# Kernel tuning notes

Hardware: AMD Instinct MI355X
Metric: run time of the kernel (lower is better)

The kernel has to match this reference:

```python
import jax, jax.numpy as jnp
from jax import lax
import numpy as np

B, W, M, F = 8, 20, 512, 16
H = 128          # n_hidden
HALF = 64        # half_hid
K = 10           # conv out channels
LONG_K = W // 2  # dilated conv kernel


def setup_inputs() -> dict:
    key = jax.random.key(0)
    ks = jax.random.split(key, 24)
    s = 0.1  # weight scale (xavier-ish)
    return {
        "X": jax.random.normal(ks[0], (B, W, M, F), jnp.float32),
        "Y": jax.random.uniform(ks[1], (B, M), jnp.float32),
        "adj": jax.random.uniform(ks[2], (M, M), jnp.float32),
        "V": jax.random.normal(ks[3], (HALF,), jnp.float32) * s,
        "bv": jax.random.normal(ks[4], (1,), jnp.float32) * s,
        "W1": jax.random.normal(ks[5], (HALF, H), jnp.float32) * s,
        "b1": jax.random.normal(ks[6], (HALF,), jnp.float32) * s,
        "W2": jax.random.normal(ks[7], (HALF, H), jnp.float32) * s,
        "Wb": jax.random.normal(ks[8], (M, M), jnp.float32) * s,
        "wb": jax.random.normal(ks[9], (1,), jnp.float32) * s,
        "conv_w": jax.random.normal(ks[10], (K, F, W), jnp.float32) * s,
        "conv_b": jax.random.normal(ks[11], (K,), jnp.float32) * s,
        "convl_w": jax.random.normal(ks[12], (K, F, LONG_K), jnp.float32) * s,
        "convl_b": jax.random.normal(ks[13], (K,), jnp.float32) * s,
        "gru_Wih": jax.random.normal(ks[14], (3 * H, F), jnp.float32) * s,
        "gru_Whh": jax.random.normal(ks[15], (3 * H, H), jnp.float32) * s,
        "gru_bih": jax.random.normal(ks[16], (3 * H,), jnp.float32) * s,
        "gru_bhh": jax.random.normal(ks[17], (3 * H,), jnp.float32) * s,
        "gc1_W": jax.random.normal(ks[18], (3 * K, H), jnp.float32) * s,
        "gc1_b": jax.random.normal(ks[19], (H,), jnp.float32) * s,
        "gc2_W": jax.random.normal(ks[20], (H, K), jnp.float32) * s,
        "gc2_b": jax.random.normal(ks[21], (K,), jnp.float32) * s,
        "out_W": jax.random.normal(ks[22], (1, H + K), jnp.float32) * s,
        "out_b": jax.random.normal(ks[23], (1,), jnp.float32) * s,
    }


def _gru_last(xseq, Wih, Whh, bih, bhh):
    # xseq: (N, T, F) -> last hidden (N, H), PyTorch GRU gate order r,z,n
    n_hid = Whh.shape[1]
    def step(h, x_t):
        gx = x_t @ Wih.T + bih
        gh = h @ Whh.T + bhh
        xr, xz, xn = jnp.split(gx, 3, axis=-1)
        hr, hz, hn = jnp.split(gh, 3, axis=-1)
        r = jax.nn.sigmoid(xr + hr)
        z = jax.nn.sigmoid(xz + hz)
        n = jnp.tanh(xn + r * hn)
        return (1.0 - z) * n + z * h, None
    h0 = jnp.zeros((xseq.shape[0], n_hid), xseq.dtype)
    hT, _ = lax.scan(step, h0, jnp.moveaxis(xseq, 1, 0))
    return hT


def _forward(X, Y, adj, V, bv, W1, b1, W2, Wb, wb, conv_w, conv_b, convl_w,
             convl_b, gru_Wih, gru_Whh, gru_bih, gru_bhh, gc1_W, gc1_b,
             gc2_W, gc2_b, out_W, out_b):
    b, w, m, f = X.shape
    # ---- temporal branch: GRU per node ----
    x = jnp.transpose(X, (0, 2, 1, 3)).reshape(b * m, w, f)
    last_hid = _gru_last(x, gru_Wih, gru_Whh, gru_bih, gru_bhh).reshape(b, m, -1)
    out_temporal = last_hid
    # ---- attention-style adaptive adjacency ----
    # hid_rpt_m[b,i,j]=last_hid[b,j]; hid_rpt_w[b,i,j]=last_hid[b,i]
    p1 = jnp.einsum('bjh,kh->bjk', last_hid, W1)  # pairs with column index j
    p2 = jnp.einsum('bih,kh->bik', last_hid, W2)  # pairs with row index i
    pre = p1[:, None, :, :] + p2[:, :, None, :] + b1  # (b,m,m,half)
    a_mx = jnp.einsum('bijk,k->bij', jax.nn.elu(pre), V) + bv[0]
    # F.normalize(p=2, dim=1)
    nrm = jnp.sqrt(jnp.sum(a_mx * a_mx, axis=1, keepdims=True))
    a_mx = a_mx / jnp.maximum(nrm, 1e-12)
    # ---- per-node conv1d (vectorized over nodes) ----
    Xc = jnp.transpose(X, (0, 2, 3, 1)).reshape(b * m, f, w)  # (bm, f, w)
    dn = ('NCH', 'OIH', 'NCH')
    r = lax.conv_general_dilated(Xc, conv_w, (1,), 'VALID', dimension_numbers=dn)
    r = r + conv_b[None, :, None]                      # (bm, K, 1)
    rl = lax.conv_general_dilated(Xc, convl_w, (1,), 'VALID',
                                  rhs_dilation=(2,), dimension_numbers=dn)
    rl = rl + convl_b[None, :, None]                   # (bm, K, long_out)
    r_cat = jnp.concatenate([r, rl], axis=-1)          # (bm, K, 1+long_out)
    r_l = jax.nn.relu(r_cat.reshape(b, m, -1))         # (b, m, (1+long_out)*K)
    # ---- gate learned adjacency with fixed adjacency ----
    c = jax.nn.sigmoid(jnp.einsum('bij,jk->bik', a_mx, Wb) + wb[0])
    A = adj[None] * c + a_mx * (1.0 - c)               # (b,m,m)
    # ---- graph convolutions: out = A @ (x @ W) + b ----
    h1 = jax.nn.relu(jnp.einsum('bij,bjh->bih', A, r_l @ gc1_W) + gc1_b)
    out_spatial = jax.nn.relu(jnp.einsum('bij,bjh->bih', A, h1 @ gc2_W) + gc2_b)
    # ---- readout ----
    out = jnp.concatenate([out_spatial, out_temporal], axis=-1)
    out = (out @ out_W.T + out_b).squeeze(-1)          # (b, m)
    y = out.reshape(-1)
    Yf = Y.reshape(-1)
    # BCE with logits: softplus(y) - Y*y, averaged
    loss = jnp.mean(jax.nn.softplus(y) - Yf * y)
    return loss, jax.nn.sigmoid(y)


def reference(X, Y, adj, V, bv, W1, b1, W2, Wb, wb, conv_w, conv_b, convl_w,
              convl_b, gru_Wih, gru_Whh, gru_bih, gru_bhh, gc1_W, gc1_b,
              gc2_W, gc2_b, out_W, out_b):
    return _forward(X, Y, adj, V, bv, W1, b1, W2, Wb, wb, conv_w, conv_b,
                    convl_w, convl_b, gru_Wih, gru_Whh, gru_bih, gru_bhh,
                    gc1_W, gc1_b, gc2_W, gc2_b, out_W, out_b)
```

## Files before the change

kernel.cpp:

```cpp
#include <hip/hip_runtime.h>
#include <math.h>

#define Bn 8
#define Wn 20
#define Mn 512
#define Fn 16
#define Hn 128
#define HALFn 64
#define Kn 10

typedef __attribute__((ext_vector_type(8))) short short8;
typedef __attribute__((ext_vector_type(4))) float f32x4;
typedef unsigned short ushort_t;

__device__ __forceinline__ float sigmoidf_(float x) {
  return 1.0f / (1.0f + __expf(-x));
}
__device__ __forceinline__ float tanhf_(float x) {
  float xx = fminf(fmaxf(x, -15.f), 15.f);
  float e = __expf(2.f * xx);
  return (e - 1.f) / (e + 1.f);
}
__device__ __forceinline__ float reluf_(float x) { return fmaxf(x, 0.f); }
__device__ __forceinline__ float eluf_(float x) {
  return (x > 0.f) ? x : (__expf(x) - 1.f);
}
__device__ __forceinline__ ushort_t bf16_rne(float v) {
  unsigned u = __float_as_uint(v);
  u += 0x7FFFu + ((u >> 16) & 1u);
  return (ushort_t)(u >> 16);
}
__device__ __forceinline__ float bf16_to_f(ushort_t b) {
  return __uint_as_float(((unsigned)b) << 16);
}

__global__ __launch_bounds__(256) void pack_kernel(
    const float* __restrict__ Whh, const float* __restrict__ Wih,
    const float* __restrict__ Wb, ushort_t* __restrict__ Bpack,
    ushort_t* __restrict__ WbT_hi, ushort_t* __restrict__ WbT_lo,
    float* __restrict__ ssq, float* __restrict__ d_out) {
  int tid = threadIdx.x;
  if (blockIdx.x < 240) {
    int idx = blockIdx.x * 256 + tid;
    if (idx < 4096) ssq[idx] = 0.f;
    if (idx == 0) d_out[0] = 0.f;
    if (idx >= 24 * 5 * 512) return;
    int j = idx & 7;
    int lane = (idx >> 3) & 63;
    int ks = (idx >> 9) % 5;
    int nt = idx / (5 * 512);
    int k = ks * 32 + (lane >> 4) * 8 + j;
    int g = (nt & 7) * 16 + (nt >> 3) * 128 + (lane & 15);
    float val = 0.f;
    if (k < 128) val = Whh[g * 128 + k];
    else if (k < 144) val = Wih[g * 16 + (k - 128)];
    ushort_t hb = bf16_rne(val);
    float lo = val - bf16_to_f(hb);
    Bpack[(((long)nt * 5 + ks) * 2 + 0) * 512 + lane * 8 + j] = hb;
    Bpack[(((long)nt * 5 + ks) * 2 + 1) * 512 + lane * 8 + j] = bf16_rne(lo);
  } else {
    int t = blockIdx.x - 240;
    int k0 = (t >> 3) * 64, j0 = (t & 7) * 64;
    __shared__ float wt[64][65];
    for (int idx = tid; idx < 4096; idx += 256) {
      int r = idx >> 6, c = idx & 63;
      wt[r][c] = Wb[(long)(k0 + r) * 512 + j0 + c];
    }
    __syncthreads();
    for (int idx = tid; idx < 4096; idx += 256) {
      int r = idx >> 6, c = idx & 63;
      float v = wt[c][r];
      ushort_t hb = bf16_rne(v);
      WbT_hi[(long)(j0 + r) * 512 + k0 + c] = hb;
      WbT_lo[(long)(j0 + r) * 512 + k0 + c] = bf16_rne(v - bf16_to_f(hb));
    }
  }
}

#define LDK 168
#define HSZ (16 * LDK)
__global__ __launch_bounds__(512, 1) void gru_kernel(
    const float* __restrict__ X, const ushort_t* __restrict__ Bpack,
    const float* __restrict__ bih, const float* __restrict__ bhh,
    const float* __restrict__ W1, const float* __restrict__ W2,
    const float* __restrict__ b1, float* __restrict__ last_hid,
    float* __restrict__ p1, float* __restrict__ p2) {
  const int tid = threadIdx.x;
  const int wave = tid >> 6;
  const int lane = tid & 63;
  const int quad = lane >> 4;
  const int jl = lane & 15;
  const int j0 = wave * 16;
  const int blk = blockIdx.x;
  const int b = blk >> 5;
  const int m0 = (blk & 31) * 16;

  __shared__ __align__(16) ushort_t smem_hs[4 * HSZ];

  short8 frR[5][2], frZ[5][2], frN[4][2], frXN[2];
#pragma unroll
  for (int ks = 0; ks < 5; ++ks) {
#pragma unroll
    for (int p = 0; p < 2; ++p) {
      frR[ks][p] = *(const short8*)&Bpack[(((long)(wave) * 5 + ks) * 2 + p) * 512 + lane * 8];
      frZ[ks][p] = *(const short8*)&Bpack[(((long)(8 + wave) * 5 + ks) * 2 + p) * 512 + lane * 8];
    }
  }
#pragma unroll
  for (int ks = 0; ks < 4; ++ks) {
#pragma unroll
    for (int p = 0; p < 2; ++p)
      frN[ks][p] = *(const short8*)&Bpack[(((long)(16 + wave) * 5 + ks) * 2 + p) * 512 + lane * 8];
  }
#pragma unroll
  for (int p = 0; p < 2; ++p)
    frXN[p] = *(const short8*)&Bpack[(((long)(16 + wave) * 5 + 4) * 2 + p) * 512 + lane * 8];

  const float cr  = bih[j0 + jl] + bhh[j0 + jl];
  const float cz  = bih[128 + j0 + jl] + bhh[128 + j0 + jl];
  const float cnx = bih[256 + j0 + jl];
  const float cnh = bhh[256 + j0 + jl];

  for (int i = tid; i < 4 * HSZ; i += 512) smem_hs[i] = 0;

  const float* Xb = X + (long)b * (Wn * Mn * Fn) + (long)m0 * Fn;
  float x0 = 0.f;
  if (tid < 256) x0 = Xb[tid];
  __syncthreads();
  if (tid < 256) {
    int s = tid >> 4, f = tid & 15;
    ushort_t hb = bf16_rne(x0);
    smem_hs[0 * HSZ + s * LDK + 128 + f] = hb;
    smem_hs[2 * HSZ + s * LDK + 128 + f] = bf16_rne(x0 - bf16_to_f(hb));
  }
  __syncthreads();

  float hp[4] = {0.f, 0.f, 0.f, 0.f};

  for (int t = 0; t < Wn; ++t) {
    const int cur = t & 1, nxt = cur ^ 1;
    const int hiC = cur * HSZ, loC = (2 + cur) * HSZ;
    const int hiN = nxt * HSZ, loN = (2 + nxt) * HSZ;
    float xpre = 0.f;
    if (tid < 256 && t < Wn - 1) xpre = Xb[(long)(t + 1) * (Mn * Fn) + tid];

    f32x4 aR[2], aZ[2], aHN[2], aXN;
    aR[0] = aR[1] = aZ[0] = aZ[1] = aHN[0] = aHN[1] = aXN = (f32x4){0.f, 0.f, 0.f, 0.f};
#pragma unroll
    for (int ks = 0; ks < 5; ++ks) {
      const int p = ks & 1;
      short8 ah = *(const short8*)&smem_hs[hiC + jl * LDK + ks * 32 + quad * 8];
      short8 al = *(const short8*)&smem_hs[loC + jl * LDK + ks * 32 + quad * 8];
      aR[p] = __builtin_amdgcn_mfma_f32_16x16x32_bf16(ah, frR[ks][0], aR[p], 0, 0, 0);
      aR[p] = __builtin_amdgcn_mfma_f32_16x16x32_bf16(ah, frR[ks][1], aR[p], 0, 0, 0);
      aR[p] = __builtin_amdgcn_mfma_f32_16x16x32_bf16(al, frR[ks][0], aR[p], 0, 0, 0);
      aZ[p] = __builtin_amdgcn_mfma_f32_16x16x32_bf16(ah, frZ[ks][0], aZ[p], 0, 0, 0);
      aZ[p] = __builtin_amdgcn_mfma_f32_16x16x32_bf16(ah, frZ[ks][1], aZ[p], 0, 0, 0);
      aZ[p] = __builtin_amdgcn_mfma_f32_16x16x32_bf16(al, frZ[ks][0], aZ[p], 0, 0, 0);
      if (ks < 4) {
        aHN[p] = __builtin_amdgcn_mfma_f32_16x16x32_bf16(ah, frN[ks][0], aHN[p], 0, 0, 0);
        aHN[p] = __builtin_amdgcn_mfma_f32_16x16x32_bf16(ah, frN[ks][1], aHN[p], 0, 0, 0);
        aHN[p] = __builtin_amdgcn_mfma_f32_16x16x32_bf16(al, frN[ks][0], aHN[p], 0, 0, 0);
      } else {
        aXN = __builtin_amdgcn_mfma_f32_16x16x32_bf16(ah, frXN[0], aXN, 0, 0, 0);
        aXN = __builtin_amdgcn_mfma_f32_16x16x32_bf16(ah, frXN[1], aXN, 0, 0, 0);
        aXN = __builtin_amdgcn_mfma_f32_16x16x32_bf16(al, frXN[0], aXN, 0, 0, 0);
      }
    }

#pragma unroll
    for (int reg = 0; reg < 4; ++reg) {
      float r = sigmoidf_(aR[0][reg] + aR[1][reg] + cr);
      float z = sigmoidf_(aZ[0][reg] + aZ[1][reg] + cz);
      float n = tanhf_(aXN[reg] + cnx + r * (aHN[0][reg] + aHN[1][reg] + cnh));
      float h = (1.f - z) * n + z * hp[reg];
      hp[reg] = h;
      int s = quad * 4 + reg;
      ushort_t hb = bf16_rne(h);
      smem_hs[hiN + s * LDK + j0 + jl] = hb;
      smem_hs[loN + s * LDK + j0 + jl] = bf16_rne(h - bf16_to_f(hb));
    }
    if (tid < 256 && t < Wn - 1) {
      int s = tid >> 4, f = tid & 15;
      ushort_t hb = bf16_rne(xpre);
      smem_hs[hiN + s * LDK + 128 + f] = hb;
      smem_hs[loN + s * LDK + 128 + f] = bf16_rne(xpre - bf16_to_f(hb));
    }
    __syncthreads();
  }

  float* hs_f = (float*)smem_hs;
#pragma unroll
  for (int reg = 0; reg < 4; ++reg) {
    int s = quad * 4 + reg;
    float h = hp[reg];
    last_hid[(long)(blk * 16 + s) * Hn + j0 + jl] = h;
    hs_f[s * 132 + j0 + jl] = h;
  }
  __syncthreads();
  {
    int k = tid & 63;
    int part = (tid >> 6) & 1;
    int sg = tid >> 7;
    const float* Wp = part ? W2 : W1;
    float a[4];
    float init = part ? 0.f : b1[k];
    a[0] = a[1] = a[2] = a[3] = init;
    for (int h = 0; h < 128; h += 4) {
      float4 w = *(const float4*)&Wp[k * 128 + h];
#pragma unroll
      for (int rr = 0; rr < 4; ++rr) {
        float4 q = *(const float4*)&hs_f[(sg * 4 + rr) * 132 + h];
        a[rr] += q.x * w.x + q.y * w.y + q.z * w.z + q.w * w.w;
      }
    }
    float* outp = part ? p2 : p1;
#pragma unroll
    for (int rr = 0; rr < 4; ++rr)
      outp[(long)(blk * 16 + sg * 4 + rr) * 64 + k] = a[rr];
  }
}

__global__ __launch_bounds__(128) void conv_t1_kernel(
    const float* __restrict__ X, const float* __restrict__ conv_w,
    const float* __restrict__ conv_b, const float* __restrict__ convl_w,
    const float* __restrict__ convl_b, const float* __restrict__ gc1_W,
    ushort_t* __restrict__ t1T_hi, ushort_t* __restrict__ t1T_lo) {
  int tid = threadIdx.x;
  int n0 = blockIdx.x * 8;
  int b = n0 >> 9, m0 = n0 & 511;
  __shared__ float xs[8][16][20];
  __shared__ float cw[3200];
  __shared__ float clw[1600];
  __shared__ float rs[8][32];
  for (int idx = tid; idx < 3200; idx += 128) cw[idx] = conv_w[idx];
  for (int idx = tid; idx < 1600; idx += 128) clw[idx] = convl_w[idx];
  for (int w = 0; w < 20; ++w)
    xs[tid >> 4][tid & 15][w] = X[((long)(b * 20 + w) * 512 + m0) * 16 + tid];
  __syncthreads();
  if (tid < 80) {
    int s = tid / 10, k = tid % 10;
    float a0 = conv_b[k];
    float l0 = convl_b[k], l1 = convl_b[k];
    for (int f = 0; f < 16; ++f) {
#pragma unroll
      for (int w = 0; w < 20; ++w) a0 = fmaf(xs[s][f][w], cw[k * 320 + f * 20 + w], a0);
#pragma unroll
      for (int q = 0; q < 10; ++q) {
        float wv = clw[k * 160 + f * 10 + q];
        l0 = fmaf(xs[s][f][2 * q], wv, l0);
        l1 = fmaf(xs[s][f][2 * q + 1], wv, l1);
      }
    }
    rs[s][k * 3 + 0] = reluf_(a0);
    rs[s][k * 3 + 1] = reluf_(l0);
    rs[s][k * 3 + 2] = reluf_(l1);
  }
  __syncthreads();
  float w[30];
#pragma unroll
  for (int q = 0; q < 30; ++q) w[q] = gc1_W[q * 128 + tid];
  long base = ((long)b * 128 + tid) * 512 + m0;
#pragma unroll
  for (int s = 0; s < 8; ++s) {
    float a = 0.f;
#pragma unroll
    for (int q = 0; q < 30; ++q) a = fmaf(rs[s][q], w[q], a);
    ushort_t hb = bf16_rne(a);
    t1T_hi[base + s] = hb;
    t1T_lo[base + s] = bf16_rne(a - bf16_to_f(hb));
  }
}

__global__ __launch_bounds__(256) void amx_kernel(
    const float* __restrict__ p1, const float* __restrict__ p2,
    const float* __restrict__ V, const float* __restrict__ bv,
    float* __restrict__ amx, float* __restrict__ ssq) {
  int tid = threadIdx.x;
  int j0 = blockIdx.x * 32, i0 = blockIdx.y * 32, bz = blockIdx.z;
  __shared__ float p1s[32][68];
  __shared__ float p2s[32][68];
  __shared__ float Vs[64];
  __shared__ float cred[16][33];
  if (tid < 64) Vs[tid] = V[tid];
  {
    int rr = tid >> 3, c0 = (tid & 7) * 8;
    *(float4*)&p1s[rr][c0]     = *(const float4*)&p1[(long)(bz * 512 + j0 + rr) * 64 + c0];
    *(float4*)&p1s[rr][c0 + 4] = *(const float4*)&p1[(long)(bz * 512 + j0 + rr) * 64 + c0 + 4];
    *(float4*)&p2s[rr][c0]     = *(const float4*)&p2[(long)(bz * 512 + i0 + rr) * 64 + c0];
    *(float4*)&p2s[rr][c0 + 4] = *(const float4*)&p2[(long)(bz * 512 + i0 + rr) * 64 + c0 + 4];
  }
  __syncthreads();
  int r0 = tid >> 4, c0 = tid & 15;
  float acc[2][2] = {{0.f, 0.f}, {0.f, 0.f}};
  for (int k = 0; k < 64; ++k) {
    float vj0 = p1s[c0][k], vj1 = p1s[c0 + 16][k];
    float vi0 = p2s[r0][k], vi1 = p2s[r0 + 16][k];
    float vk = Vs[k];
    acc[0][0] = fmaf(eluf_(vj0 + vi0), vk, acc[0][0]);
    acc[0][1] = fmaf(eluf_(vj1 + vi0), vk, acc[0][1]);
    acc[1][0] = fmaf(eluf_(vj0 + vi1), vk, acc[1][0]);
    acc[1][1] = fmaf(eluf_(vj1 + vi1), vk, acc[1][1]);
  }
  float bvv = bv[0];
  float s2[2] = {0.f, 0.f};
#pragma unroll
  for (int a = 0; a < 2; ++a)
#pragma unroll
    for (int c = 0; c < 2; ++c) {
      float v = acc[a][c] + bvv;
      amx[((long)(bz * 512 + i0 + r0 + a * 16)) * 512 + j0 + c0 + c * 16] = v;
      s2[c] += v * v;
    }
  cred[r0][c0] = s2[0];
  cred[r0][c0 + 16] = s2[1];
  __syncthreads();
  if (tid < 32) {
    float s = 0.f;
#pragma unroll
    for (int p = 0; p < 16; ++p) s += cred[p][tid];
    atomicAdd(&ssq[bz * 512 + j0 + tid], s);
  }
}

#define CPK 40
__global__ __launch_bounds__(256, 2) void gemm_cA(
    const float* __restrict__ amx, const ushort_t* __restrict__ WbT_hi,
    const ushort_t* __restrict__ WbT_lo, const float* __restrict__ adj,
    const float* __restrict__ wb, const float* __restrict__ ssq,
    float* __restrict__ A) {
  const int bz = blockIdx.z;
  const int i0 = blockIdx.y * 64;
  const int j0 = blockIdx.x * 64;
  const int tid = threadIdx.x;
  const int wave = tid >> 6;
  const int lane = tid & 63;
  const int quad = lane >> 4, jl = lane & 15;
  const int wm = (wave & 1) * 32, wn = (wave >> 1) * 32;

  __shared__ __align__(16) ushort_t Ahi[64][CPK];
  __shared__ __align__(16) ushort_t Alo[64][CPK];
  __shared__ __align__(16) ushort_t Bhi[64][CPK];
  __shared__ __align__(16) ushort_t Blo[64][CPK];
  __shared__ float rs_s[512];

  const float* Abase = amx + (long)bz * 262144;
  const float* sb = ssq + bz * 512;
  for (int i = tid; i < 512; i += 256)
    rs_s[i] = 1.f / fmaxf(sqrtf(sb[i]), 1e-12f);

  f32x4 acc[2][2];
#pragma unroll
  for (int a = 0; a < 2; ++a)
#pragma unroll
    for (int c = 0; c < 2; ++c) acc[a][c] = (f32x4){0.f, 0.f, 0.f, 0.f};

  for (int kk0 = 0; kk0 < 512; kk0 += 32) {
    __syncthreads();
#pragma unroll
    for (int l = 0; l < 2; ++l) {
      int e = l * 1024 + tid * 4;
      int r = e >> 5, kq = e & 31;
      float4 v = *(const float4*)&Abase[(long)(i0 + r) * 512 + kk0 + kq];
      float4 sc = *(const float4*)&rs_s[kk0 + kq];
      float vv[4] = {v.x * sc.x, v.y * sc.y, v.z * sc.z, v.w * sc.w};
#pragma unroll
      for (int q = 0; q < 4; ++q) {
        ushort_t hb = bf16_rne(vv[q]);
        Ahi[r][kq + q] = hb;
        Alo[r][kq + q] = bf16_rne(vv[q] - bf16_to_f(hb));
      }
    }
    {
      int r = tid >> 2, kc = (tid & 3) * 8;
      *(uint4*)&Bhi[r][kc] = *(const uint4*)&WbT_hi[(long)(j0 + r) * 512 + kk0 + kc];
      *(uint4*)&Blo[r][kc] = *(const uint4*)&WbT_lo[(long)(j0 + r) * 512 + kk0 + kc];
    }
    __syncthreads();
    short8 ah[2], al[2], bh[2], bl[2];
#pragma unroll
    for (int tm = 0; tm < 2; ++tm) {
      ah[tm] = *(const short8*)&Ahi[wm + tm * 16 + jl][quad * 8];
      al[tm] = *(const short8*)&Alo[wm + tm * 16 + jl][quad * 8];
    }
#pragma unroll
    for (int tn = 0; tn < 2; ++tn) {
      bh[tn] = *(const short8*)&Bhi[wn + tn * 16 + jl][quad * 8];
      bl[tn] = *(const short8*)&Blo[wn + tn * 16 + jl][quad * 8];
    }
#pragma unroll
    for (int tm = 0; tm < 2; ++tm)
#pragma unroll
      for (int tn = 0; tn < 2; ++tn) {
        acc[tm][tn] = __builtin_amdgcn_mfma_f32_16x16x32_bf16(ah[tm], bh[tn], acc[tm][tn], 0, 0, 0);
        acc[tm][tn] = __builtin_amdgcn_mfma_f32_16x16x32_bf16(ah[tm], bl[tn], acc[tm][tn], 0, 0, 0);
        acc[tm][tn] = __builtin_amdgcn_mfma_f32_16x16x32_bf16(al[tm], bh[tn], acc[tm][tn], 0, 0, 0);
      }
  }

  const float wbv = wb[0];
#pragma unroll
  for (int tn = 0; tn < 2; ++tn) {
    int j = j0 + wn + tn * 16 + jl;
    float sj = rs_s[j];
#pragma unroll
    for (int tm = 0; tm < 2; ++tm) {
#pragma unroll
      for (int reg = 0; reg < 4; ++reg) {
        int i = i0 + wm + tm * 16 + quad * 4 + reg;
        long ofs = (long)bz * 262144 + (long)i * 512 + j;
        float c = sigmoidf_(acc[tm][tn][reg] + wbv);
        float am = Abase[(long)i * 512 + j] * sj;
        float ad = adj[(long)i * 512 + j];
        A[ofs] = ad * c + am * (1.f - c);
      }
    }
  }
}

__global__ __launch_bounds__(512, 1) void gemm_h1t2(
    const float* __restrict__ A, const ushort_t* __restrict__ t1T_hi,
    const ushort_t* __restrict__ t1T_lo, const float* __restrict__ gc1_b,
    const float* __restrict__ gc2_W, float* __restrict__ t2) {
  const int bz = blockIdx.y;
  const int i0 = blockIdx.x * 16;
  const int tid = threadIdx.x;
  const int wave = tid >> 6;
  const int lane = tid & 63;
  const int quad = lane >> 4, jl = lane & 15;

  __shared__ __align__(16) ushort_t Ahi[16][CPK];
  __shared__ __align__(16) ushort_t Alo[16][CPK];
  __shared__ __align__(16) ushort_t Bhi[128][CPK];
  __shared__ __align__(16) ushort_t Blo[128][CPK];
  __shared__ float h1s[16][132];
  __shared__ float gw[1280];

  const float* Ab = A + (long)bz * 262144;
  for (int idx = tid; idx < 1280; idx += 512) gw[idx] = gc2_W[idx];

  f32x4 acc = {0.f, 0.f, 0.f, 0.f};

  for (int kk0 = 0; kk0 < 512; kk0 += 32) {
    __syncthreads();
    {
      int r = tid >> 5, kq = tid & 31;
      float v = Ab[(long)(i0 + r) * 512 + kk0 + kq];
      ushort_t hb = bf16_rne(v);
      Ahi[r][kq] = hb;
      Alo[r][kq] = bf16_rne(v - bf16_to_f(hb));
    }
    {
      int r = tid >> 2, kc = (tid & 3) * 8;
      *(uint4*)&Bhi[r][kc] = *(const uint4*)&t1T_hi[((long)bz * 128 + r) * 512 + kk0 + kc];
      *(uint4*)&Blo[r][kc] = *(const uint4*)&t1T_lo[((long)bz * 128 + r) * 512 + kk0 + kc];
    }
    __syncthreads();
    short8 ah = *(const short8*)&Ahi[jl][quad * 8];
    short8 al = *(const short8*)&Alo[jl][quad * 8];
    short8 bh = *(const short8*)&Bhi[wave * 16 + jl][quad * 8];
    short8 bl = *(const short8*)&Blo[wave * 16 + jl][quad * 8];
    acc = __builtin_amdgcn_mfma_f32_16x16x32_bf16(ah, bh, acc, 0, 0, 0);
    acc = __builtin_amdgcn_mfma_f32_16x16x32_bf16(ah, bl, acc, 0, 0, 0);
    acc = __builtin_amdgcn_mfma_f32_16x16x32_bf16(al, bh, acc, 0, 0, 0);
  }
  __syncthreads();
  {
    int n = wave * 16 + jl;
    float bb = gc1_b[n];
#pragma unroll
    for (int reg = 0; reg < 4; ++reg) {
      int r = quad * 4 + reg;
      h1s[r][n] = reluf_(acc[reg] + bb);
    }
  }
  __syncthreads();
  if (tid < 160) {
    int r = tid / 10, c = tid % 10;
    float a = 0.f;
#pragma unroll 4
    for (int k = 0; k < 128; ++k) a = fmaf(h1s[r][k], gw[k * 10 + c], a);
    t2[((long)bz * 512 + i0 + r) * 10 + c] = a;
  }
}

__global__ __launch_bounds__(256) void spat_readout(
    const float* __restrict__ A, const float* __restrict__ t2,
    const float* __restrict__ gc2_b, const float* __restrict__ last_hid,
    const float* __restrict__ out_W, const float* __restrict__ out_b,
    const float* __restrict__ Y, float* __restrict__ d_out) {
  int tid = threadIdx.x;
  int bz = blockIdx.y;
  int i0 = blockIdx.x * 8;
  __shared__ float t2s[5120];
  __shared__ float wS[138];
  __shared__ float osps[8][12];
  for (int idx = tid; idx < 5120; idx += 256) t2s[idx] = t2[(long)bz * 5120 + idx];
  for (int idx = tid; idx < 138; idx += 256) wS[idx] = out_W[idx];
  __syncthreads();
  int r = tid >> 5, sk = tid & 31;
  const float* Arow = A + (long)bz * 262144 + (long)(i0 + r) * 512;
  float acc[10] = {0, 0, 0, 0, 0, 0, 0, 0, 0, 0};
  for (int k = sk; k < 512; k += 32) {
    float av = Arow[k];
    const float* tp = &t2s[k * 10];
#pragma unroll
    for (int c = 0; c < 10; ++c) acc[c] = fmaf(av, tp[c], acc[c]);
  }
#pragma unroll
  for (int off = 16; off; off >>= 1)
#pragma unroll
    for (int c = 0; c < 10; ++c) acc[c] += __shfl_xor(acc[c], off);
  if (sk == 0) {
#pragma unroll
    for (int c = 0; c < 10; ++c) osps[r][c] = reluf_(acc[c] + gc2_b[c]);
  }
  __syncthreads();
  float l = 0.f;
  if (tid < 8) {
    int gid = bz * 512 + i0 + tid;
    float y = out_b[0];
#pragma unroll
    for (int k = 0; k < 10; ++k) y = fmaf(osps[tid][k], wS[k], y);
    const float* hp = &last_hid[(long)gid * 128];
    for (int h = 0; h < 128; h += 4) {
      float4 hv = *(const float4*)&hp[h];
      y = fmaf(hv.x, wS[10 + h + 0], y);
      y = fmaf(hv.y, wS[10 + h + 1], y);
      y = fmaf(hv.z, wS[10 + h + 2], y);
      y = fmaf(hv.w, wS[10 + h + 3], y);
    }
    d_out[1 + gid] = sigmoidf_(y);
    l = fmaxf(y, 0.f) + log1pf(__expf(-fabsf(y))) - Y[gid] * y;
  }
  if (tid < 64) {
#pragma unroll
    for (int off = 4; off; off >>= 1) l += __shfl_down(l, off);
    if (tid == 0) atomicAdd(d_out, l * (1.0f / 4096.f));
  }
}

extern "C" void kernel_launch(void* const* d_in, const int* in_sizes, int n_in,
                              void* d_out, int out_size, void* d_ws, size_t ws_size,
                              hipStream_t stream) {
  const float* X       = (const float*)d_in[0];
  const float* Y       = (const float*)d_in[1];
  const float* adj     = (const float*)d_in[2];
  const float* V       = (const float*)d_in[3];
  const float* bv      = (const float*)d_in[4];
  const float* W1      = (const float*)d_in[5];
  const float* b1      = (const float*)d_in[6];
  const float* W2      = (const float*)d_in[7];
  const float* Wb      = (const float*)d_in[8];
  const float* wb      = (const float*)d_in[9];
  const float* conv_w  = (const float*)d_in[10];
  const float* conv_b  = (const float*)d_in[11];
  const float* convl_w = (const float*)d_in[12];
  const float* convl_b = (const float*)d_in[13];
  const float* gWih    = (const float*)d_in[14];
  const float* gWhh    = (const float*)d_in[15];
  const float* gbih    = (const float*)d_in[16];
  const float* gbhh    = (const float*)d_in[17];
  const float* gc1_W   = (const float*)d_in[18];
  const float* gc1_b   = (const float*)d_in[19];
  const float* gc2_W   = (const float*)d_in[20];
  const float* gc2_b   = (const float*)d_in[21];
  const float* out_W   = (const float*)d_in[22];
  const float* out_b   = (const float*)d_in[23];
  float* out = (float*)d_out;

  float* ws = (float*)d_ws;
  float* lhid  = ws; ws += 524288;
  float* p1    = ws; ws += 262144;
  float* p2    = ws; ws += 262144;
  float* amx   = ws; ws += 2097152;
  float* ssq   = ws; ws += 4096;
  float* Abuf  = ws; ws += 2097152;
  float* t2    = ws; ws += 40960;
  float* Bpkf  = ws; ws += 122880;
  float* WbTf  = ws; ws += 262144;
  float* t1Tf  = ws; ws += 524288;
  if (ws_size < (size_t)(ws - (float*)d_ws) * sizeof(float)) return;
  ushort_t* Bpack  = (ushort_t*)Bpkf;
  ushort_t* WbT_hi = (ushort_t*)WbTf;
  ushort_t* WbT_lo = WbT_hi + 262144;
  ushort_t* t1T_hi = (ushort_t*)t1Tf;
  ushort_t* t1T_lo = t1T_hi + 524288;

  pack_kernel<<<304, 256, 0, stream>>>(gWhh, gWih, Wb, Bpack, WbT_hi, WbT_lo,
                                       ssq, out);
  gru_kernel<<<256, 512, 0, stream>>>(X, Bpack, gbih, gbhh, W1, W2, b1,
                                      lhid, p1, p2);
  conv_t1_kernel<<<512, 128, 0, stream>>>(X, conv_w, conv_b, convl_w, convl_b,
                                          gc1_W, t1T_hi, t1T_lo);
  amx_kernel<<<dim3(16, 16, 8), 256, 0, stream>>>(p1, p2, V, bv, amx, ssq);
  gemm_cA<<<dim3(8, 8, 8), 256, 0, stream>>>(amx, WbT_hi, WbT_lo, adj, wb,
                                             ssq, Abuf);
  gemm_h1t2<<<dim3(32, 8), 512, 0, stream>>>(Abuf, t1T_hi, t1T_lo, gc1_b,
                                             gc2_W, t2);
  spat_readout<<<dim3(64, 8), 256, 0, stream>>>(Abuf, t2, gc2_b, lhid,
                                                out_W, out_b, Y, out);
}
```

Before: 256.1 us.

## Fuse pack, conv and amx kernels; pack GRU weight fragments inside the GRU kernel

Drops the separate pack kernel. The GRU kernel now loads Whh/Wih rows and splits them into bf16 hi/lo fragments itself. The conv/t1, amx and Wb transpose work is merged into one mid_kernel, where each block computes a full column strip of amx so it can write the inverse norm scale directly instead of using atomics into ssq. This cuts kernel launches and per-launch gaps. The cost is less parallelism in the amx phase and serialised phases within each block.

```diff
diff --git a/kernel.cpp b/kernel.cpp
--- a/kernel.cpp
+++ b/kernel.cpp
@@ -6,8 +6,6 @@
 #define Mn 512
 #define Fn 16
 #define Hn 128
-#define HALFn 64
-#define Kn 10
 
 typedef __attribute__((ext_vector_type(8))) short short8;
 typedef __attribute__((ext_vector_type(4))) float f32x4;
@@ -33,58 +31,49 @@
 __device__ __forceinline__ float bf16_to_f(ushort_t b) {
   return __uint_as_float(((unsigned)b) << 16);
 }
-
-__global__ __launch_bounds__(256) void pack_kernel(
+__device__ __forceinline__ void split8(const float v[8], short8& hi, short8& lo) {
+#pragma unroll
+  for (int j = 0; j < 8; ++j) {
+    ushort_t h = bf16_rne(v[j]);
+    hi[j] = (short)h;
+    lo[j] = (short)bf16_rne(v[j] - bf16_to_f(h));
+  }
+}
+__device__ __forceinline__ void load_gate_frags(
     const float* __restrict__ Whh, const float* __restrict__ Wih,
-    const float* __restrict__ Wb, ushort_t* __restrict__ Bpack,
-    ushort_t* __restrict__ WbT_hi, ushort_t* __restrict__ WbT_lo,
-    float* __restrict__ ssq, float* __restrict__ d_out) {
-  int tid = threadIdx.x;
-  if (blockIdx.x < 240) {
-    int idx = blockIdx.x * 256 + tid;
-    if (idx < 4096) ssq[idx] = 0.f;
-    if (idx == 0) d_out[0] = 0.f;
-    if (idx >= 24 * 5 * 512) return;
-    int j = idx & 7;
-    int lane = (idx >> 3) & 63;
-    int ks = (idx >> 9) % 5;
-    int nt = idx / (5 * 512);
-    int k = ks * 32 + (lane >> 4) * 8 + j;
-    int g = (nt & 7) * 16 + (nt >> 3) * 128 + (lane & 15);
-    float val = 0.f;
-    if (k < 128) val = Whh[g * 128 + k];
-    else if (k < 144) val = Wih[g * 16 + (k - 128)];
-    ushort_t hb = bf16_rne(val);
-    float lo = val - bf16_to_f(hb);
-    Bpack[(((long)nt * 5 + ks) * 2 + 0) * 512 + lane * 8 + j] = hb;
-    Bpack[(((long)nt * 5 + ks) * 2 + 1) * 512 + lane * 8 + j] = bf16_rne(lo);
-  } else {
-    int t = blockIdx.x - 240;
-    int k0 = (t >> 3) * 64, j0 = (t & 7) * 64;
-    __shared__ float wt[64][65];
-    for (int idx = tid; idx < 4096; idx += 256) {
-      int r = idx >> 6, c = idx & 63;
-      wt[r][c] = Wb[(long)(k0 + r) * 512 + j0 + c];
-    }
-    __syncthreads();
-    for (int idx = tid; idx < 4096; idx += 256) {
-      int r = idx >> 6, c = idx & 63;
-      float v = wt[c][r];
-      ushort_t hb = bf16_rne(v);
-      WbT_hi[(long)(j0 + r) * 512 + k0 + c] = hb;
-      WbT_lo[(long)(j0 + r) * 512 + k0 + c] = bf16_rne(v - bf16_to_f(hb));
-    }
+    int row, int quad, short8 fr[5][2]) {
+  const float* wrow = Whh + (long)row * 128;
+#pragma unroll
+  for (int ks = 0; ks < 4; ++ks) {
+    float v[8];
+    float4 a4 = *(const float4*)&wrow[ks * 32 + quad * 8];
+    float4 b4 = *(const float4*)&wrow[ks * 32 + quad * 8 + 4];
+    v[0] = a4.x; v[1] = a4.y; v[2] = a4.z; v[3] = a4.w;
+    v[4] = b4.x; v[5] = b4.y; v[6] = b4.z; v[7] = b4.w;
+    split8(v, fr[ks][0], fr[ks][1]);
+  }
+  {
+    float v[8] = {0.f, 0.f, 0.f, 0.f, 0.f, 0.f, 0.f, 0.f};
+    if (quad < 2) {
+      const float* xrow = Wih + (long)row * 16;
+      float4 a4 = *(const float4*)&xrow[quad * 8];
+      float4 b4 = *(const float4*)&xrow[quad * 8 + 4];
+      v[0] = a4.x; v[1] = a4.y; v[2] = a4.z; v[3] = a4.w;
+      v[4] = b4.x; v[5] = b4.y; v[6] = b4.z; v[7] = b4.w;
+    }
+    split8(v, fr[4][0], fr[4][1]);
   }
 }
 
 #define LDK 168
 #define HSZ (16 * LDK)
 __global__ __launch_bounds__(512, 1) void gru_kernel(
-    const float* __restrict__ X, const ushort_t* __restrict__ Bpack,
-    const float* __restrict__ bih, const float* __restrict__ bhh,
-    const float* __restrict__ W1, const float* __restrict__ W2,
-    const float* __restrict__ b1, float* __restrict__ last_hid,
-    float* __restrict__ p1, float* __restrict__ p2) {
+    const float* __restrict__ X, const float* __restrict__ Whh,
+    const float* __restrict__ Wih, const float* __restrict__ bih,
+    const float* __restrict__ bhh, const float* __restrict__ W1,
+    const float* __restrict__ W2, const float* __restrict__ b1,
+    float* __restrict__ last_hid, float* __restrict__ p1,
+    float* __restrict__ p2, float* __restrict__ d_out) {
   const int tid = threadIdx.x;
   const int wave = tid >> 6;
   const int lane = tid & 63;
@@ -95,26 +84,14 @@
   const int b = blk >> 5;
   const int m0 = (blk & 31) * 16;
 
+  if (blk == 0 && tid == 0) d_out[0] = 0.f;
+
   __shared__ __align__(16) ushort_t smem_hs[4 * HSZ];
 
-  short8 frR[5][2], frZ[5][2], frN[4][2], frXN[2];
-#pragma unroll
-  for (int ks = 0; ks < 5; ++ks) {
-#pragma unroll
-    for (int p = 0; p < 2; ++p) {
-      frR[ks][p] = *(const short8*)&Bpack[(((long)(wave) * 5 + ks) * 2 + p) * 512 + lane * 8];
-      frZ[ks][p] = *(const short8*)&Bpack[(((long)(8 + wave) * 5 + ks) * 2 + p) * 512 + lane * 8];
-    }
-  }
-#pragma unroll
-  for (int ks = 0; ks < 4; ++ks) {
-#pragma unroll
-    for (int p = 0; p < 2; ++p)
-      frN[ks][p] = *(const short8*)&Bpack[(((long)(16 + wave) * 5 + ks) * 2 + p) * 512 + lane * 8];
-  }
-#pragma unroll
-  for (int p = 0; p < 2; ++p)
-    frXN[p] = *(const short8*)&Bpack[(((long)(16 + wave) * 5 + 4) * 2 + p) * 512 + lane * 8];
+  short8 frR[5][2], frZ[5][2], frN[5][2];
+  load_gate_frags(Whh, Wih, wave * 16 + jl, quad, frR);
+  load_gate_frags(Whh, Wih, 128 + wave * 16 + jl, quad, frZ);
+  load_gate_frags(Whh, Wih, 256 + wave * 16 + jl, quad, frN);
 
   const float cr  = bih[j0 + jl] + bhh[j0 + jl];
   const float cz  = bih[128 + j0 + jl] + bhh[128 + j0 + jl];
@@ -162,9 +139,9 @@
         aHN[p] = __builtin_amdgcn_mfma_f32_16x16x32_bf16(ah, frN[ks][1], aHN[p], 0, 0, 0);
         aHN[p] = __builtin_amdgcn_mfma_f32_16x16x32_bf16(al, frN[ks][0], aHN[p], 0, 0, 0);
       } else {
-        aXN = __builtin_amdgcn_mfma_f32_16x16x32_bf16(ah, frXN[0], aXN, 0, 0, 0);
-        aXN = __builtin_amdgcn_mfma_f32_16x16x32_bf16(ah, frXN[1], aXN, 0, 0, 0);
-        aXN = __builtin_amdgcn_mfma_f32_16x16x32_bf16(al, frXN[0], aXN, 0, 0, 0);
+        aXN = __builtin_amdgcn_mfma_f32_16x16x32_bf16(ah, frN[4][0], aXN, 0, 0, 0);
+        aXN = __builtin_amdgcn_mfma_f32_16x16x32_bf16(ah, frN[4][1], aXN, 0, 0, 0);
+        aXN = __builtin_amdgcn_mfma_f32_16x16x32_bf16(al, frN[4][0], aXN, 0, 0, 0);
       }
     }
 
@@ -221,105 +198,126 @@
   }
 }
 
-__global__ __launch_bounds__(128) void conv_t1_kernel(
+__global__ __launch_bounds__(256) void mid_kernel(
     const float* __restrict__ X, const float* __restrict__ conv_w,
     const float* __restrict__ conv_b, const float* __restrict__ convl_w,
     const float* __restrict__ convl_b, const float* __restrict__ gc1_W,
-    ushort_t* __restrict__ t1T_hi, ushort_t* __restrict__ t1T_lo) {
-  int tid = threadIdx.x;
-  int n0 = blockIdx.x * 8;
-  int b = n0 >> 9, m0 = n0 & 511;
-  __shared__ float xs[8][16][20];
-  __shared__ float cw[3200];
-  __shared__ float clw[1600];
-  __shared__ float rs[8][32];
-  for (int idx = tid; idx < 3200; idx += 128) cw[idx] = conv_w[idx];
-  for (int idx = tid; idx < 1600; idx += 128) clw[idx] = convl_w[idx];
-  for (int w = 0; w < 20; ++w)
-    xs[tid >> 4][tid & 15][w] = X[((long)(b * 20 + w) * 512 + m0) * 16 + tid];
-  __syncthreads();
-  if (tid < 80) {
-    int s = tid / 10, k = tid % 10;
-    float a0 = conv_b[k];
-    float l0 = convl_b[k], l1 = convl_b[k];
-    for (int f = 0; f < 16; ++f) {
-#pragma unroll
-      for (int w = 0; w < 20; ++w) a0 = fmaf(xs[s][f][w], cw[k * 320 + f * 20 + w], a0);
-#pragma unroll
-      for (int q = 0; q < 10; ++q) {
-        float wv = clw[k * 160 + f * 10 + q];
-        l0 = fmaf(xs[s][f][2 * q], wv, l0);
-        l1 = fmaf(xs[s][f][2 * q + 1], wv, l1);
-      }
-    }
-    rs[s][k * 3 + 0] = reluf_(a0);
-    rs[s][k * 3 + 1] = reluf_(l0);
-    rs[s][k * 3 + 2] = reluf_(l1);
-  }
-  __syncthreads();
-  float w[30];
-#pragma unroll
-  for (int q = 0; q < 30; ++q) w[q] = gc1_W[q * 128 + tid];
-  long base = ((long)b * 128 + tid) * 512 + m0;
-#pragma unroll
-  for (int s = 0; s < 8; ++s) {
-    float a = 0.f;
-#pragma unroll
-    for (int q = 0; q < 30; ++q) a = fmaf(rs[s][q], w[q], a);
-    ushort_t hb = bf16_rne(a);
-    t1T_hi[base + s] = hb;
-    t1T_lo[base + s] = bf16_rne(a - bf16_to_f(hb));
-  }
-}
-
-__global__ __launch_bounds__(256) void amx_kernel(
     const float* __restrict__ p1, const float* __restrict__ p2,
     const float* __restrict__ V, const float* __restrict__ bv,
-    float* __restrict__ amx, float* __restrict__ ssq) {
-  int tid = threadIdx.x;
-  int j0 = blockIdx.x * 32, i0 = blockIdx.y * 32, bz = blockIdx.z;
-  __shared__ float p1s[32][68];
-  __shared__ float p2s[32][68];
-  __shared__ float Vs[64];
-  __shared__ float cred[16][33];
-  if (tid < 64) Vs[tid] = V[tid];
+    const float* __restrict__ Wb, ushort_t* __restrict__ t1T_hi,
+    ushort_t* __restrict__ t1T_lo, ushort_t* __restrict__ WbT_hi,
+    ushort_t* __restrict__ WbT_lo, float* __restrict__ amx,
+    float* __restrict__ scl) {
+  int tid = threadIdx.x, blk = blockIdx.x;
+  __shared__ __align__(16) char sm[30720];
+
   {
-    int rr = tid >> 3, c0 = (tid & 7) * 8;
-    *(float4*)&p1s[rr][c0]     = *(const float4*)&p1[(long)(bz * 512 + j0 + rr) * 64 + c0];
-    *(float4*)&p1s[rr][c0 + 4] = *(const float4*)&p1[(long)(bz * 512 + j0 + rr) * 64 + c0 + 4];
-    *(float4*)&p2s[rr][c0]     = *(const float4*)&p2[(long)(bz * 512 + i0 + rr) * 64 + c0];
-    *(float4*)&p2s[rr][c0 + 4] = *(const float4*)&p2[(long)(bz * 512 + i0 + rr) * 64 + c0 + 4];
-  }
-  __syncthreads();
-  int r0 = tid >> 4, c0 = tid & 15;
-  float acc[2][2] = {{0.f, 0.f}, {0.f, 0.f}};
-  for (int k = 0; k < 64; ++k) {
-    float vj0 = p1s[c0][k], vj1 = p1s[c0 + 16][k];
-    float vi0 = p2s[r0][k], vi1 = p2s[r0 + 16][k];
-    float vk = Vs[k];
-    acc[0][0] = fmaf(eluf_(vj0 + vi0), vk, acc[0][0]);
-    acc[0][1] = fmaf(eluf_(vj1 + vi0), vk, acc[0][1]);
-    acc[1][0] = fmaf(eluf_(vj0 + vi1), vk, acc[1][0]);
-    acc[1][1] = fmaf(eluf_(vj1 + vi1), vk, acc[1][1]);
-  }
-  float bvv = bv[0];
-  float s2[2] = {0.f, 0.f};
-#pragma unroll
-  for (int a = 0; a < 2; ++a)
-#pragma unroll
-    for (int c = 0; c < 2; ++c) {
-      float v = acc[a][c] + bvv;
-      amx[((long)(bz * 512 + i0 + r0 + a * 16)) * 512 + j0 + c0 + c * 16] = v;
-      s2[c] += v * v;
-    }
-  cred[r0][c0] = s2[0];
-  cred[r0][c0 + 16] = s2[1];
-  __syncthreads();
-  if (tid < 32) {
-    float s = 0.f;
-#pragma unroll
-    for (int p = 0; p < 16; ++p) s += cred[p][tid];
-    atomicAdd(&ssq[bz * 512 + j0 + tid], s);
+    float* xs  = (float*)sm;
+    float* cw  = (float*)(sm + 10240);
+    float* clw = (float*)(sm + 23040);
+    float* rs  = (float*)(sm + 29440);
+    int n0 = blk * 8, b = n0 >> 9, m0 = n0 & 511;
+    for (int idx = tid; idx < 3200; idx += 256) cw[idx] = conv_w[idx];
+    for (int idx = tid; idx < 1600; idx += 256) clw[idx] = convl_w[idx];
+    if (tid < 128) {
+      for (int w = 0; w < 20; ++w)
+        xs[tid * 20 + w] = X[((long)(b * 20 + w) * 512 + m0) * 16 + tid];
+    }
+    __syncthreads();
+    if (tid < 80) {
+      int s = tid / 10, k = tid % 10;
+      float a0 = conv_b[k];
+      float l0 = convl_b[k], l1 = convl_b[k];
+      for (int f = 0; f < 16; ++f) {
+        const float* xp = &xs[(s * 16 + f) * 20];
+#pragma unroll
+        for (int w = 0; w < 20; ++w) a0 = fmaf(xp[w], cw[k * 320 + f * 20 + w], a0);
+#pragma unroll
+        for (int q = 0; q < 10; ++q) {
+          float wv = clw[k * 160 + f * 10 + q];
+          l0 = fmaf(xp[2 * q], wv, l0);
+          l1 = fmaf(xp[2 * q + 1], wv, l1);
+        }
+      }
+      rs[s * 32 + k * 3 + 0] = reluf_(a0);
+      rs[s * 32 + k * 3 + 1] = reluf_(l0);
+      rs[s * 32 + k * 3 + 2] = reluf_(l1);
+    }
+    __syncthreads();
+    if (tid < 128) {
+      float w[30];
+#pragma unroll
+      for (int q = 0; q < 30; ++q) w[q] = gc1_W[q * 128 + tid];
+      long base = ((long)b * 128 + tid) * 512 + m0;
+#pragma unroll
+      for (int s = 0; s < 8; ++s) {
+        float a = 0.f;
+#pragma unroll
+        for (int q = 0; q < 30; ++q) a = fmaf(rs[s * 32 + q], w[q], a);
+        ushort_t hb = bf16_rne(a);
+        t1T_hi[base + s] = hb;
+        t1T_lo[base + s] = bf16_rne(a - bf16_to_f(hb));
+      }
+    }
+  }
+  __syncthreads();
+
+  {
+    float* Vs   = (float*)sm;
+    float* p1s  = (float*)(sm + 256);
+    float* p2s  = (float*)(sm + 2432);
+    float* sred = (float*)(sm + 11136);
+    int j0 = (blk & 63) * 8, bz = blk >> 6;
+    if (tid < 64) Vs[tid] = V[tid];
+    for (int idx = tid; idx < 512; idx += 256) {
+      int r = idx >> 6, k = idx & 63;
+      p1s[r * 68 + k] = p1[(long)(bz * 512 + j0 + r) * 64 + k];
+    }
+    float bvv = bv[0];
+    int r = tid >> 3, c = tid & 7;
+    float ss = 0.f;
+    for (int it = 0; it < 16; ++it) {
+      int i0 = it * 32;
+      __syncthreads();
+      for (int idx = tid; idx < 2048; idx += 256) {
+        int rr = idx >> 6, k = idx & 63;
+        p2s[rr * 68 + k] = p2[(long)(bz * 512 + i0 + rr) * 64 + k];
+      }
+      __syncthreads();
+      float acc = 0.f;
+#pragma unroll 4
+      for (int k = 0; k < 64; ++k)
+        acc = fmaf(eluf_(p1s[c * 68 + k] + p2s[r * 68 + k]), Vs[k], acc);
+      float v = acc + bvv;
+      amx[((long)(bz * 512 + i0 + r)) * 512 + j0 + c] = v;
+      ss += v * v;
+    }
+    sred[r * 8 + c] = ss;
+    __syncthreads();
+    if (tid < 8) {
+      float s = 0.f;
+#pragma unroll
+      for (int p = 0; p < 32; ++p) s += sred[p * 8 + tid];
+      scl[bz * 512 + j0 + tid] = 1.f / fmaxf(sqrtf(s), 1e-12f);
+    }
+  }
+
+  if (blk < 64) {
+    __syncthreads();
+    float* wt = (float*)sm;
+    int k0 = (blk >> 3) * 64, j0w = (blk & 7) * 64;
+    for (int idx = tid; idx < 4096; idx += 256) {
+      int r = idx >> 6, c = idx & 63;
+      wt[r * 65 + c] = Wb[(long)(k0 + r) * 512 + j0w + c];
+    }
+    __syncthreads();
+    for (int idx = tid; idx < 4096; idx += 256) {
+      int r = idx >> 6, c = idx & 63;
+      float v = wt[c * 65 + r];
+      ushort_t hb = bf16_rne(v);
+      WbT_hi[(long)(j0w + r) * 512 + k0 + c] = hb;
+      WbT_lo[(long)(j0w + r) * 512 + k0 + c] = bf16_rne(v - bf16_to_f(hb));
+    }
   }
 }
 
@@ -327,7 +325,7 @@
 __global__ __launch_bounds__(256, 2) void gemm_cA(
     const float* __restrict__ amx, const ushort_t* __restrict__ WbT_hi,
     const ushort_t* __restrict__ WbT_lo, const float* __restrict__ adj,
-    const float* __restrict__ wb, const float* __restrict__ ssq,
+    const float* __restrict__ wb, const float* __restrict__ scl,
     float* __restrict__ A) {
   const int bz = blockIdx.z;
   const int i0 = blockIdx.y * 64;
@@ -345,9 +343,7 @@
   __shared__ float rs_s[512];
 
   const float* Abase = amx + (long)bz * 262144;
-  const float* sb = ssq + bz * 512;
-  for (int i = tid; i < 512; i += 256)
-    rs_s[i] = 1.f / fmaxf(sqrtf(sb[i]), 1e-12f);
+  for (int i = tid; i < 512; i += 256) rs_s[i] = scl[bz * 512 + i];
 
   f32x4 acc[2][2];
 #pragma unroll
@@ -574,28 +570,24 @@
   float* p1    = ws; ws += 262144;
   float* p2    = ws; ws += 262144;
   float* amx   = ws; ws += 2097152;
-  float* ssq   = ws; ws += 4096;
+  float* scl   = ws; ws += 4096;
   float* Abuf  = ws; ws += 2097152;
   float* t2    = ws; ws += 40960;
-  float* Bpkf  = ws; ws += 122880;
   float* WbTf  = ws; ws += 262144;
   float* t1Tf  = ws; ws += 524288;
   if (ws_size < (size_t)(ws - (float*)d_ws) * sizeof(float)) return;
-  ushort_t* Bpack  = (ushort_t*)Bpkf;
   ushort_t* WbT_hi = (ushort_t*)WbTf;
   ushort_t* WbT_lo = WbT_hi + 262144;
   ushort_t* t1T_hi = (ushort_t*)t1Tf;
   ushort_t* t1T_lo = t1T_hi + 524288;
 
-  pack_kernel<<<304, 256, 0, stream>>>(gWhh, gWih, Wb, Bpack, WbT_hi, WbT_lo,
-                                       ssq, out);
-  gru_kernel<<<256, 512, 0, stream>>>(X, Bpack, gbih, gbhh, W1, W2, b1,
-                                      lhid, p1, p2);
-  conv_t1_kernel<<<512, 128, 0, stream>>>(X, conv_w, conv_b, convl_w, convl_b,
-                                          gc1_W, t1T_hi, t1T_lo);
-  amx_kernel<<<dim3(16, 16, 8), 256, 0, stream>>>(p1, p2, V, bv, amx, ssq);
+  gru_kernel<<<256, 512, 0, stream>>>(X, gWhh, gWih, gbih, gbhh, W1, W2, b1,
+                                      lhid, p1, p2, out);
+  mid_kernel<<<512, 256, 0, stream>>>(X, conv_w, conv_b, convl_w, convl_b,
+                                      gc1_W, p1, p2, V, bv, Wb,
+                                      t1T_hi, t1T_lo, WbT_hi, WbT_lo, amx, scl);
   gemm_cA<<<dim3(8, 8, 8), 256, 0, stream>>>(amx, WbT_hi, WbT_lo, adj, wb,
-                                             ssq, Abuf);
+                                             scl, Abuf);
   gemm_h1t2<<<dim3(32, 8), 512, 0, stream>>>(Abuf, t1T_hi, t1T_lo, gc1_b,
                                              gc2_W, t2);
   spat_readout<<<dim3(64, 8), 256, 0, stream>>>(Abuf, t2, gc2_b, lhid,
```

New measurement: 273.3 us. +6.7%, slower.
